# Kernel tuning notes

Measured on AMD Instinct MI355X. Metric: run time of the kernel, lower is better.

The kernel has to match this reference:

```python
import jax, jax.numpy as jnp
import numpy as np

G, N, E, K, D = 32768, 128, 1024, 32, 3
B = G // 2


def setup_inputs() -> dict:
    key = jax.random.key(0)
    ks = jax.random.split(key, 12)
    x = jax.random.normal(ks[0], (G, N, D), dtype=jnp.float32)
    edge_src = jax.random.randint(ks[1], (G, E), 0, N, dtype=jnp.int32)
    edge_dst = jax.random.randint(ks[2], (G, E), 0, N, dtype=jnp.int32)
    ext_x = jax.random.normal(ks[3], (G, K, D), dtype=jnp.float32)
    # xavier-normal-ish 3x3 params
    s = float(np.sqrt(2.0 / (D + D)))
    W = jax.random.normal(ks[4], (D, D), dtype=jnp.float32) * s
    M = jax.random.normal(ks[5], (D, D), dtype=jnp.float32) * s
    U = jax.random.normal(ks[6], (D, D), dtype=jnp.float32) * s
    V = jax.random.normal(ks[7], (D, D), dtype=jnp.float32) * s
    # link-prediction MLP (Linear(6,3), Linear(3,2))
    W1 = jax.random.uniform(ks[8], (2 * D, D), dtype=jnp.float32, minval=-1, maxval=1) / np.sqrt(2 * D)
    b1 = jnp.zeros((D,), dtype=jnp.float32)
    W2 = jax.random.uniform(ks[9], (D, 2), dtype=jnp.float32, minval=-1, maxval=1) / np.sqrt(D)
    b2 = jnp.zeros((2,), dtype=jnp.float32)
    return {"x": x, "edge_src": edge_src, "edge_dst": edge_dst, "ext_x": ext_x,
            "W": W, "M": M, "U": U, "V": V, "W1": W1, "b1": b1, "W2": W2, "b2": b2}


def _neigh_sum(xg, src, dst):
    # gather source node reps and scatter-add into destination nodes: [N, D]
    return jax.ops.segment_sum(xg[src], dst, num_segments=N)


def reference(x, edge_src, edge_dst, ext_x, W, M, U, V, W1, b1, W2, b2):
    # InternalGraphConvolutionLayer: h = relu(x@W + (sum of neighbour reps)@M)
    agg = jax.vmap(_neigh_sum)(x, edge_src, edge_dst)          # [G, N, D]
    h = jax.nn.relu(jnp.einsum('gnd,de->gne', x, W) +
                    jnp.einsum('gnd,de->gne', agg, M))          # [G, N, D]
    emb = jax.nn.softmax(h.sum(axis=1), axis=-1)                # [G, D]
    # ExternalGraphConvolutionLayer: relu(emb@U + sum_k ext_x@V), softmax
    ext = jax.nn.relu(emb @ U + ext_x.sum(axis=1) @ V)          # [G, D]
    g_emb = jax.nn.softmax(ext, axis=-1)                        # [G, D]
    # LinkPredictionLayer on graph pairs
    e1, e2 = g_emb[:B], g_emb[B:]                               # [B, D] each
    t = jnp.concatenate([e1 * e2, e1 + e2], axis=1)             # [B, 2D]
    hlp = jax.nn.relu(t @ W1 + b1)                              # [B, D]
    out = jax.nn.softmax(hlp @ W2 + b2, axis=-1)                # [B, 2]
    return out
```

## Files before the change

kernel.cpp:

```cpp
#include <hip/hip_runtime.h>

#define NG    32768
#define NN    128
#define NE    1024
#define NK    32
#define NB    (NG / 2)
#define RSTR  17
#define AWDW  (NN * RSTR)

__global__ __launch_bounds__(256) void dcnn_adj_kernel(
    const float* __restrict__ x,
    const int*   __restrict__ esrc,
    const int*   __restrict__ edst,
    const float* __restrict__ extx,
    const float* __restrict__ W,
    const float* __restrict__ M,
    const float* __restrict__ U,
    const float* __restrict__ V,
    const float* __restrict__ W1,
    const float* __restrict__ b1,
    const float* __restrict__ W2,
    const float* __restrict__ b2,
    float* __restrict__ out)
{
    __shared__ unsigned A[4 * AWDW];
    __shared__ float ge[4][3];

    const int t    = threadIdx.x;
    const int w    = t >> 6;
    const int lane = t & 63;
    const int pair = blockIdx.x * 2 + (w >> 1);
    const int g    = (w & 1) ? (pair + NB) : pair;

    const float* __restrict__ xg = x + (size_t)g * (NN * 3);

    const int4* sp = (const int4*)(esrc + (size_t)g * NE);
    const int4* dp = (const int4*)(edst + (size_t)g * NE);
    const int4 s0 = sp[lane], s1 = sp[lane + 64], s2 = sp[lane + 128], s3 = sp[lane + 192];
    const int4 d0 = dp[lane], d1 = dp[lane + 64], d2 = dp[lane + 128], d3 = dp[lane + 192];

    float er0 = 0.f, er1 = 0.f, er2 = 0.f;
    if (lane < NK) {
        const float* ep = extx + (size_t)g * (NK * 3) + lane * 3;
        er0 = ep[0]; er1 = ep[1]; er2 = ep[2];
    }

    unsigned* Aw = &A[w * AWDW];
    #pragma unroll
    for (int i = 0; i < 34; ++i) {
        const int idx = i * 64 + lane;
        if (idx < AWDW) Aw[idx] = 0u;
    }

    __builtin_amdgcn_wave_barrier();

    #define SCAT(SV, DV)                                                    \
        {                                                                   \
            const unsigned off = (unsigned)(size_t)&Aw[(DV) * RSTR + ((SV) >> 3)]; \
            const unsigned val = 1u << (4 * ((SV) & 7));                    \
            asm volatile("ds_add_u32 %0, %1" :: "v"(off), "v"(val) : "memory"); \
        }
    SCAT(s0.x, d0.x) SCAT(s0.y, d0.y) SCAT(s0.z, d0.z) SCAT(s0.w, d0.w)
    SCAT(s1.x, d1.x) SCAT(s1.y, d1.y) SCAT(s1.z, d1.z) SCAT(s1.w, d1.w)
    SCAT(s2.x, d2.x) SCAT(s2.y, d2.y) SCAT(s2.z, d2.z) SCAT(s2.w, d2.w)
    SCAT(s3.x, d3.x) SCAT(s3.y, d3.y) SCAT(s3.z, d3.z) SCAT(s3.w, d3.w)
    #undef SCAT

    asm volatile("s_waitcnt lgkmcnt(0)" ::: "memory");
    __builtin_amdgcn_wave_barrier();

    float ac0 = 0.f, ac1 = 0.f, ac2 = 0.f;
    float ac3 = 0.f, ac4 = 0.f, ac5 = 0.f;
    const int r0 = lane * RSTR;
    const int r1 = (lane + 64) * RSTR;

    #pragma unroll
    for (int j = 0; j < 16; ++j) {
        const unsigned da = Aw[r0 + j];
        const unsigned db = Aw[r1 + j];
        float q[24];
        *(float4*)&q[0]  = *(const float4*)(xg + j * 24);
        *(float4*)&q[4]  = *(const float4*)(xg + j * 24 + 4);
        *(float4*)&q[8]  = *(const float4*)(xg + j * 24 + 8);
        *(float4*)&q[12] = *(const float4*)(xg + j * 24 + 12);
        *(float4*)&q[16] = *(const float4*)(xg + j * 24 + 16);
        *(float4*)&q[20] = *(const float4*)(xg + j * 24 + 20);
        #pragma unroll
        for (int o = 0; o < 8; ++o) {
            const float ca = (float)((da >> (4 * o)) & 15u);
            const float cb = (float)((db >> (4 * o)) & 15u);
            const float xs0 = q[o * 3], xs1 = q[o * 3 + 1], xs2 = q[o * 3 + 2];
            ac0 += ca * xs0; ac1 += ca * xs1; ac2 += ca * xs2;
            ac3 += cb * xs0; ac4 += cb * xs1; ac5 += cb * xs2;
        }
    }

    float h0, h1, h2;
    {
        const float* xr = xg + lane * 3;
        const float x0 = xr[0], x1 = xr[1], x2 = xr[2];
        h0 = fmaxf(x0 * W[0] + x1 * W[3] + x2 * W[6] +
                   ac0 * M[0] + ac1 * M[3] + ac2 * M[6], 0.f);
        h1 = fmaxf(x0 * W[1] + x1 * W[4] + x2 * W[7] +
                   ac0 * M[1] + ac1 * M[4] + ac2 * M[7], 0.f);
        h2 = fmaxf(x0 * W[2] + x1 * W[5] + x2 * W[8] +
                   ac0 * M[2] + ac1 * M[5] + ac2 * M[8], 0.f);
    }
    {
        const float* xr = xg + (lane + 64) * 3;
        const float x0 = xr[0], x1 = xr[1], x2 = xr[2];
        h0 += fmaxf(x0 * W[0] + x1 * W[3] + x2 * W[6] +
                    ac3 * M[0] + ac4 * M[3] + ac5 * M[6], 0.f);
        h1 += fmaxf(x0 * W[1] + x1 * W[4] + x2 * W[7] +
                    ac3 * M[1] + ac4 * M[4] + ac5 * M[7], 0.f);
        h2 += fmaxf(x0 * W[2] + x1 * W[5] + x2 * W[8] +
                    ac3 * M[2] + ac4 * M[5] + ac5 * M[8], 0.f);
    }

    #pragma unroll
    for (int off = 16; off > 0; off >>= 1) {
        h0  += __shfl_xor(h0,  off);
        h1  += __shfl_xor(h1,  off);
        h2  += __shfl_xor(h2,  off);
        er0 += __shfl_xor(er0, off);
        er1 += __shfl_xor(er1, off);
        er2 += __shfl_xor(er2, off);
    }
    #define RL(v) (__uint_as_float(__builtin_amdgcn_readlane(__float_as_uint(v), 0)) + \
                   __uint_as_float(__builtin_amdgcn_readlane(__float_as_uint(v), 32)))
    const float H0 = RL(h0), H1 = RL(h1), H2 = RL(h2);
    const float E0 = RL(er0), E1 = RL(er1), E2 = RL(er2);
    #undef RL

    if (lane == 0) {
        const float mx = fmaxf(H0, fmaxf(H1, H2));
        const float e0 = __expf(H0 - mx), e1 = __expf(H1 - mx), e2 = __expf(H2 - mx);
        const float inv = 1.0f / (e0 + e1 + e2);
        const float emb0 = e0 * inv, emb1 = e1 * inv, emb2 = e2 * inv;

        float ext[3];
        #pragma unroll
        for (int e = 0; e < 3; ++e) {
            const float vv = emb0 * U[e] + emb1 * U[3 + e] + emb2 * U[6 + e]
                           + E0   * V[e] + E1   * V[3 + e] + E2   * V[6 + e];
            ext[e] = fmaxf(vv, 0.f);
        }
        const float mx2 = fmaxf(ext[0], fmaxf(ext[1], ext[2]));
        const float f0 = __expf(ext[0] - mx2), f1 = __expf(ext[1] - mx2), f2 = __expf(ext[2] - mx2);
        const float inv2 = 1.0f / (f0 + f1 + f2);
        ge[w][0] = f0 * inv2; ge[w][1] = f1 * inv2; ge[w][2] = f2 * inv2;
    }

    __syncthreads();

    if ((w & 1) == 0 && lane == 0) {
        float tt[6];
        tt[0] = ge[w][0] * ge[w + 1][0];
        tt[1] = ge[w][1] * ge[w + 1][1];
        tt[2] = ge[w][2] * ge[w + 1][2];
        tt[3] = ge[w][0] + ge[w + 1][0];
        tt[4] = ge[w][1] + ge[w + 1][1];
        tt[5] = ge[w][2] + ge[w + 1][2];

        float hl[3];
        #pragma unroll
        for (int j = 0; j < 3; ++j) {
            float vv = b1[j];
            #pragma unroll
            for (int i = 0; i < 6; ++i) vv += tt[i] * W1[i * 3 + j];
            hl[j] = fmaxf(vv, 0.f);
        }

        const float l0 = b2[0] + hl[0] * W2[0] + hl[1] * W2[2] + hl[2] * W2[4];
        const float l1 = b2[1] + hl[0] * W2[1] + hl[1] * W2[3] + hl[2] * W2[5];
        const float mm = fmaxf(l0, l1);
        const float q0 = __expf(l0 - mm), q1 = __expf(l1 - mm);
        const float qi = 1.0f / (q0 + q1);
        out[(size_t)pair * 2    ] = q0 * qi;
        out[(size_t)pair * 2 + 1] = q1 * qi;
    }
}

extern "C" void kernel_launch(void* const* d_in, const int* in_sizes, int n_in,
                              void* d_out, int out_size, void* d_ws, size_t ws_size,
                              hipStream_t stream) {
    const float* x    = (const float*)d_in[0];
    const int*   esrc = (const int*)  d_in[1];
    const int*   edst = (const int*)  d_in[2];
    const float* extx = (const float*)d_in[3];
    const float* W    = (const float*)d_in[4];
    const float* M    = (const float*)d_in[5];
    const float* U    = (const float*)d_in[6];
    const float* V    = (const float*)d_in[7];
    const float* W1   = (const float*)d_in[8];
    const float* b1   = (const float*)d_in[9];
    const float* W2   = (const float*)d_in[10];
    const float* b2   = (const float*)d_in[11];
    float* out = (float*)d_out;

    dcnn_adj_kernel<<<NB / 2, 256, 0, stream>>>(
        x, esrc, edst, extx, W, M, U, V, W1, b1, W2, b2, out);
}
```

Baseline: 394.3 us.

## Replace packed adjacency-count matrix with direct float scatter-add of neighbour features

Instead of building a 4-bit packed adjacency count matrix in LDS and then doing a dense 128x128 matrix-vector pass over x, each wave stages x into LDS and scatter-adds the gathered source features into a per-node float accumulator with ds_add_f32. This removes the dense reconstruction loop and the repeated global reads of x, at the cost of three LDS float atomics per edge instead of one integer atomic. It also adds a min-waves-per-EU launch bound. Summation order changes, so float results may differ slightly.

After: 756.6 us. 91.9% more time.

```diff
diff --git a/kernel.cpp b/kernel.cpp
--- a/kernel.cpp
+++ b/kernel.cpp
@@ -5,10 +5,8 @@
 #define NE    1024
 #define NK    32
 #define NB    (NG / 2)
-#define RSTR  17
-#define AWDW  (NN * RSTR)
 
-__global__ __launch_bounds__(256) void dcnn_adj_kernel(
+__global__ __launch_bounds__(256, 6) void dcnn_adj_kernel(
     const float* __restrict__ x,
     const int*   __restrict__ esrc,
     const int*   __restrict__ edst,
@@ -23,7 +21,8 @@
     const float* __restrict__ b2,
     float* __restrict__ out)
 {
-    __shared__ unsigned A[4 * AWDW];
+    __shared__ __attribute__((aligned(16))) float xs[4][NN][4];
+    __shared__ __attribute__((aligned(16))) float ag[4][NN][4];
     __shared__ float ge[4][3];
 
     const int t    = threadIdx.x;
@@ -45,77 +44,71 @@
         er0 = ep[0]; er1 = ep[1]; er2 = ep[2];
     }
 
-    unsigned* Aw = &A[w * AWDW];
-    #pragma unroll
-    for (int i = 0; i < 34; ++i) {
-        const int idx = i * 64 + lane;
-        if (idx < AWDW) Aw[idx] = 0u;
-    }
+    float* __restrict__ xw = &xs[w][0][0];
+    float* __restrict__ aw = &ag[w][0][0];
+
+    const float* p0 = xg + lane * 3;
+    const float v0 = p0[0], v1 = p0[1], v2 = p0[2];
+    const float* p1 = xg + (lane + 64) * 3;
+    const float u0 = p1[0], u1 = p1[1], u2 = p1[2];
+
+    *(float4*)&xw[lane * 4]        = make_float4(v0, v1, v2, 0.f);
+    *(float4*)&xw[(lane + 64) * 4] = make_float4(u0, u1, u2, 0.f);
+    const float4 z4 = make_float4(0.f, 0.f, 0.f, 0.f);
+    *(float4*)&aw[lane * 4]        = z4;
+    *(float4*)&aw[(lane + 64) * 4] = z4;
 
     __builtin_amdgcn_wave_barrier();
 
-    #define SCAT(SV, DV)                                                    \
-        {                                                                   \
-            const unsigned off = (unsigned)(size_t)&Aw[(DV) * RSTR + ((SV) >> 3)]; \
-            const unsigned val = 1u << (4 * ((SV) & 7));                    \
-            asm volatile("ds_add_u32 %0, %1" :: "v"(off), "v"(val) : "memory"); \
+    #define CHUNK(SA, DA)                                                       \
+        {                                                                       \
+            const float4 xa = *(const float4*)&xw[(SA).x * 4];                  \
+            const float4 xb = *(const float4*)&xw[(SA).y * 4];                  \
+            const float4 xc = *(const float4*)&xw[(SA).z * 4];                  \
+            const float4 xd = *(const float4*)&xw[(SA).w * 4];                  \
+            const unsigned oa = (unsigned)(size_t)&aw[(DA).x * 4];              \
+            const unsigned ob = (unsigned)(size_t)&aw[(DA).y * 4];              \
+            const unsigned oc = (unsigned)(size_t)&aw[(DA).z * 4];              \
+            const unsigned od = (unsigned)(size_t)&aw[(DA).w * 4];              \
+            asm volatile("ds_add_f32 %0, %1"          :: "v"(oa), "v"(xa.x) : "memory"); \
+            asm volatile("ds_add_f32 %0, %1 offset:4" :: "v"(oa), "v"(xa.y) : "memory"); \
+            asm volatile("ds_add_f32 %0, %1 offset:8" :: "v"(oa), "v"(xa.z) : "memory"); \
+            asm volatile("ds_add_f32 %0, %1"          :: "v"(ob), "v"(xb.x) : "memory"); \
+            asm volatile("ds_add_f32 %0, %1 offset:4" :: "v"(ob), "v"(xb.y) : "memory"); \
+            asm volatile("ds_add_f32 %0, %1 offset:8" :: "v"(ob), "v"(xb.z) : "memory"); \
+            asm volatile("ds_add_f32 %0, %1"          :: "v"(oc), "v"(xc.x) : "memory"); \
+            asm volatile("ds_add_f32 %0, %1 offset:4" :: "v"(oc), "v"(xc.y) : "memory"); \
+            asm volatile("ds_add_f32 %0, %1 offset:8" :: "v"(oc), "v"(xc.z) : "memory"); \
+            asm volatile("ds_add_f32 %0, %1"          :: "v"(od), "v"(xd.x) : "memory"); \
+            asm volatile("ds_add_f32 %0, %1 offset:4" :: "v"(od), "v"(xd.y) : "memory"); \
+            asm volatile("ds_add_f32 %0, %1 offset:8" :: "v"(od), "v"(xd.z) : "memory"); \
         }
-    SCAT(s0.x, d0.x) SCAT(s0.y, d0.y) SCAT(s0.z, d0.z) SCAT(s0.w, d0.w)
-    SCAT(s1.x, d1.x) SCAT(s1.y, d1.y) SCAT(s1.z, d1.z) SCAT(s1.w, d1.w)
-    SCAT(s2.x, d2.x) SCAT(s2.y, d2.y) SCAT(s2.z, d2.z) SCAT(s2.w, d2.w)
-    SCAT(s3.x, d3.x) SCAT(s3.y, d3.y) SCAT(s3.z, d3.z) SCAT(s3.w, d3.w)
-    #undef SCAT
+    CHUNK(s0, d0)
+    CHUNK(s1, d1)
+    CHUNK(s2, d2)
+    CHUNK(s3, d3)
+    #undef CHUNK
 
     asm volatile("s_waitcnt lgkmcnt(0)" ::: "memory");
     __builtin_amdgcn_wave_barrier();
 
-    float ac0 = 0.f, ac1 = 0.f, ac2 = 0.f;
-    float ac3 = 0.f, ac4 = 0.f, ac5 = 0.f;
-    const int r0 = lane * RSTR;
-    const int r1 = (lane + 64) * RSTR;
-
-    #pragma unroll
-    for (int j = 0; j < 16; ++j) {
-        const unsigned da = Aw[r0 + j];
-        const unsigned db = Aw[r1 + j];
-        float q[24];
-        *(float4*)&q[0]  = *(const float4*)(xg + j * 24);
-        *(float4*)&q[4]  = *(const float4*)(xg + j * 24 + 4);
-        *(float4*)&q[8]  = *(const float4*)(xg + j * 24 + 8);
-        *(float4*)&q[12] = *(const float4*)(xg + j * 24 + 12);
-        *(float4*)&q[16] = *(const float4*)(xg + j * 24 + 16);
-        *(float4*)&q[20] = *(const float4*)(xg + j * 24 + 20);
-        #pragma unroll
-        for (int o = 0; o < 8; ++o) {
-            const float ca = (float)((da >> (4 * o)) & 15u);
-            const float cb = (float)((db >> (4 * o)) & 15u);
-            const float xs0 = q[o * 3], xs1 = q[o * 3 + 1], xs2 = q[o * 3 + 2];
-            ac0 += ca * xs0; ac1 += ca * xs1; ac2 += ca * xs2;
-            ac3 += cb * xs0; ac4 += cb * xs1; ac5 += cb * xs2;
-        }
-    }
+    const float4 A0 = *(const float4*)&aw[lane * 4];
+    const float4 A1 = *(const float4*)&aw[(lane + 64) * 4];
 
     float h0, h1, h2;
-    {
-        const float* xr = xg + lane * 3;
-        const float x0 = xr[0], x1 = xr[1], x2 = xr[2];
-        h0 = fmaxf(x0 * W[0] + x1 * W[3] + x2 * W[6] +
-                   ac0 * M[0] + ac1 * M[3] + ac2 * M[6], 0.f);
-        h1 = fmaxf(x0 * W[1] + x1 * W[4] + x2 * W[7] +
-                   ac0 * M[1] + ac1 * M[4] + ac2 * M[7], 0.f);
-        h2 = fmaxf(x0 * W[2] + x1 * W[5] + x2 * W[8] +
-                   ac0 * M[2] + ac1 * M[5] + ac2 * M[8], 0.f);
-    }
-    {
-        const float* xr = xg + (lane + 64) * 3;
-        const float x0 = xr[0], x1 = xr[1], x2 = xr[2];
-        h0 += fmaxf(x0 * W[0] + x1 * W[3] + x2 * W[6] +
-                    ac3 * M[0] + ac4 * M[3] + ac5 * M[6], 0.f);
-        h1 += fmaxf(x0 * W[1] + x1 * W[4] + x2 * W[7] +
-                    ac3 * M[1] + ac4 * M[4] + ac5 * M[7], 0.f);
-        h2 += fmaxf(x0 * W[2] + x1 * W[5] + x2 * W[8] +
-                    ac3 * M[2] + ac4 * M[5] + ac5 * M[8], 0.f);
-    }
+    h0 = fmaxf(v0 * W[0] + v1 * W[3] + v2 * W[6] +
+               A0.x * M[0] + A0.y * M[3] + A0.z * M[6], 0.f);
+    h1 = fmaxf(v0 * W[1] + v1 * W[4] + v2 * W[7] +
+               A0.x * M[1] + A0.y * M[4] + A0.z * M[7], 0.f);
+    h2 = fmaxf(v0 * W[2] + v1 * W[5] + v2 * W[8] +
+               A0.x * M[2] + A0.y * M[5] + A0.z * M[8], 0.f);
+
+    h0 += fmaxf(u0 * W[0] + u1 * W[3] + u2 * W[6] +
+                A1.x * M[0] + A1.y * M[3] + A1.z * M[6], 0.f);
+    h1 += fmaxf(u0 * W[1] + u1 * W[4] + u2 * W[7] +
+                A1.x * M[1] + A1.y * M[4] + A1.z * M[7], 0.f);
+    h2 += fmaxf(u0 * W[2] + u1 * W[5] + u2 * W[8] +
+                A1.x * M[2] + A1.y * M[5] + A1.z * M[8], 0.f);
 
     #pragma unroll
     for (int off = 16; off > 0; off >>= 1) {
```
